# Kernel optimization log

Hardware: AMD Instinct MI355X
Metric: run time of the kernel (lower is better)

## Reference

```python
import jax, jax.numpy as jnp
import numpy as np

B, N, DIM, HEADS = 1, 4096, 1024, 16
HEAD_DIM = DIM // HEADS
SCALE = HEAD_DIM ** -0.5
GRID = 64  # GRID*GRID == N, power-of-2 Hilbert grid


def _hilbert_d2xy(n, d):
    # standard Hilbert curve distance->(x,y), vectorized in numpy
    rx = np.zeros_like(d)
    ry = np.zeros_like(d)
    x = np.zeros_like(d)
    y = np.zeros_like(d)
    t = d.copy()
    s = 1
    while s < n:
        rx = (t // 2) & 1
        ry = (t ^ rx) & 1
        # rotate
        swap = ry == 0
        flip = swap & (rx == 1)
        x_f = np.where(flip, s - 1 - x, x)
        y_f = np.where(flip, s - 1 - y, y)
        x, y = np.where(swap, y_f, x_f), np.where(swap, x_f, y_f)
        x = x + s * rx
        y = y + s * ry
        t = t // 4
        s *= 2
    return x, y


def _hilbert_indices(n_tokens, grid):
    d = np.arange(n_tokens)
    hx, hy = _hilbert_d2xy(grid, d)
    # token at Hilbert distance d lives at row-major position hy*grid+hx
    return (hy * grid + hx).astype(np.int32)


def setup_inputs() -> dict:
    key = jax.random.key(0)
    k1, k2, k3 = jax.random.split(key, 3)
    x = jax.random.normal(k1, (B, N, DIM), dtype=jnp.float32)
    w_qkv = jax.random.normal(k2, (3 * DIM, DIM), dtype=jnp.float32) * (DIM ** -0.5)
    w_out = jax.random.normal(k3, (DIM, DIM), dtype=jnp.float32) * (DIM ** -0.5)
    indices = jnp.asarray(_hilbert_indices(N, GRID))
    return {"x": x, "w_qkv": w_qkv, "w_out": w_out, "indices": indices}


def reference(x, w_qkv, w_out, indices):
    b, n, c = x.shape
    # qkv projection: nn.Linear -> x @ W^T, reshape to [B,N,3,H,Dh]
    qkv = jnp.einsum("bnc,dc->bnd", x, w_qkv).reshape(b, n, 3, HEADS, HEAD_DIM)
    q, k, v = qkv[:, :, 0], qkv[:, :, 1], qkv[:, :, 2]  # each [B,N,H,Dh]
    # Hilbert gather along sequence
    q = q[:, indices]
    k = k[:, indices]
    v = v[:, indices]
    # full softmax attention per head
    scores = jnp.einsum("bnhd,bmhd->bhnm", q, k) * SCALE
    attn = jax.nn.softmax(scores, axis=-1)
    out = jnp.einsum("bhnm,bmhd->bnhd", attn, v)  # [B,N,H,Dh]
    # scatter back to original order
    inv = jnp.argsort(indices)
    out = out[:, inv].reshape(b, n, c)
    return jnp.einsum("bnc,dc->bnd", out, w_out)
```

## Files before the change

kernel.cpp:

```cpp
#include <hip/hip_runtime.h>
#include <stdint.h>

#define NTOK 4096
#define HD 64
#define DIMC 1024

typedef __attribute__((ext_vector_type(8))) short s16x8;
typedef __attribute__((ext_vector_type(4))) float f32x4;

#if __has_builtin(__builtin_amdgcn_exp2f)
#define EXP2(x) __builtin_amdgcn_exp2f(x)
#else
#define EXP2(x) exp2f(x)
#endif

__device__ inline unsigned short f2bf(float f) {
  union { float f; unsigned u; } v; v.f = f;
  unsigned r = v.u + 0x7FFFu + ((v.u >> 16) & 1u);
  return (unsigned short)(r >> 16);
}

__device__ inline unsigned cvt_pk_bf16(float lo, float hi) {
  unsigned r;
  asm("v_cvt_pk_bf16_f32 %0, %1, %2" : "=v"(r) : "v"(lo), "v"(hi));
  return r;
}

__device__ inline float bf2f(unsigned short u) {
  union { unsigned u; float f; } v; v.u = ((unsigned)u) << 16;
  return v.f;
}

__device__ inline void gld16(const void* g, void* s) {
  __builtin_amdgcn_global_load_lds((const __attribute__((address_space(1))) void*)g,
                                   (__attribute__((address_space(3))) void*)s, 16, 0, 0);
}

#define N4_X   1048576
#define N4_WQ  786432
__global__ void cvt_all(const float4* __restrict__ x, const float4* __restrict__ wq,
                        ushort4* __restrict__ xb, ushort4* __restrict__ wqb) {
  int i = blockIdx.x * 256 + threadIdx.x;
  const float4* s; ushort4* d; int off;
  if (i < N4_X) { s = x; d = xb; off = i; }
  else { s = wq; d = wqb; off = i - N4_X; }
  float4 v = s[off];
  ushort4 o;
  o.x = f2bf(v.x); o.y = f2bf(v.y); o.z = f2bf(v.z); o.w = f2bf(v.w);
  d[off] = o;
}

#define QSCALE 0.18033688011112042f
__global__ __launch_bounds__(256) void gemm_qkv(
    const unsigned short* __restrict__ A,
    const unsigned short* __restrict__ B,
    unsigned short* __restrict__ qb,
    unsigned short* __restrict__ kb,
    unsigned short* __restrict__ vtb)
{
  __shared__ unsigned short As[128 * 32];
  __shared__ unsigned short Bs[128 * 32];
  const int t = threadIdx.x;
  const int l = t & 63;
  const int w = t >> 6;
  const int wr = w >> 1, wc = w & 1;
  const int bm = blockIdx.x, bn = blockIdx.y;
  const int K = 1024;

  f32x4 acc[4][4];
#pragma unroll
  for (int m = 0; m < 4; ++m)
#pragma unroll
    for (int n = 0; n < 4; ++n)
#pragma unroll
      for (int r = 0; r < 4; ++r) acc[m][n][r] = 0.f;

  for (int kt = 0; kt < K; kt += 32) {
    __syncthreads();
#pragma unroll
    for (int j = 0; j < 2; ++j) {
      const int o = j * 4096 + t * 16;
      const int row = o >> 6;
      const int cole = (o & 63) >> 1;
      gld16(A + (size_t)(bm * 128 + row) * K + kt + cole, (char*)As + o);
      gld16(B + (size_t)(bn * 128 + row) * K + kt + cole, (char*)Bs + o);
    }
    __syncthreads();
    s16x8 af[4], bfr[4];
    const int cb = (l >> 4) * 16;
#pragma unroll
    for (int m = 0; m < 4; ++m)
      af[m] = *(const s16x8*)((const char*)As + (wr * 64 + m * 16 + (l & 15)) * 64 + cb);
#pragma unroll
    for (int n = 0; n < 4; ++n)
      bfr[n] = *(const s16x8*)((const char*)Bs + (wc * 64 + n * 16 + (l & 15)) * 64 + cb);
#pragma unroll
    for (int m = 0; m < 4; ++m)
#pragma unroll
      for (int n = 0; n < 4; ++n)
        acc[m][n] = __builtin_amdgcn_mfma_f32_16x16x32_bf16(af[m], bfr[n], acc[m][n], 0, 0, 0);
  }

#pragma unroll
  for (int m = 0; m < 4; ++m) {
#pragma unroll
    for (int n = 0; n < 4; ++n) {
#pragma unroll
      for (int r = 0; r < 4; ++r) {
        const int gm = bm * 128 + wr * 64 + m * 16 + (l >> 4) * 4 + r;
        const int gn = bn * 128 + wc * 64 + n * 16 + (l & 15);
        const float val = acc[m][n][r];
        const int part = gn >> 10;
        const int h = (gn >> 6) & 15;
        const int dd = gn & 63;
        if (part == 0)      qb[((size_t)h * NTOK + gm) * HD + dd] = f2bf(val * QSCALE);
        else if (part == 1) kb[((size_t)h * NTOK + gm) * HD + dd] = f2bf(val);
        else                vtb[((size_t)h * HD + dd) * NTOK + gm] = f2bf(val);
      }
    }
  }
}

__global__ __launch_bounds__(128, 4) void fa_split(
    const unsigned short* __restrict__ Q,
    const unsigned short* __restrict__ Kin,
    const unsigned short* __restrict__ Vt,
    unsigned short* __restrict__ Opart,
    float* __restrict__ Lpart)
{
  __shared__ unsigned short Ks[2][32 * 64];
  __shared__ unsigned short Vs[2][64 * 32];

  const int t = threadIdx.x, l = t & 63, w = t >> 6;
  const int g = l >> 4, q = l & 15;
  const int wg = blockIdx.x;
  const int h = wg & 15;
  const int qt = (wg >> 4) & 63;
  const int half = wg >> 10;
  const int q0 = qt * 64 + w * 32;
  const int kbase0 = half * (NTOK / 2);
  const unsigned short* Qh = Q + (size_t)h * NTOK * HD;
  const unsigned short* Kh = Kin + (size_t)h * NTOK * HD;
  const unsigned short* Vh = Vt + (size_t)h * HD * NTOK;

  int offK[2], offV[2];
#pragma unroll
  for (int j = 0; j < 2; ++j) {
    const int o = j * 2048 + t * 16;
    const int rho = o >> 7;
    const int c = o & 127;
    const int n = ((rho & 12) << 1) | ((rho & 16) >> 2) | (rho & 3);
    offK[j] = n * 128 + (c ^ ((rho & 7) << 4));
    const int rv = o >> 6;
    const int cv = o & 63;
    offV[j] = rv * (NTOK * 2) + (cv ^ (((rv >> 1) & 3) << 4));
  }

  s16x8 qf[2][2];
#pragma unroll
  for (int rb = 0; rb < 2; ++rb)
#pragma unroll
    for (int tq = 0; tq < 2; ++tq)
      qf[rb][tq] = *(const s16x8*)(Qh + (size_t)(q0 + rb * 16 + q) * HD + tq * 32 + g * 8);

  s16x8 ones;
#pragma unroll
  for (int i = 0; i < 8; ++i) ones[i] = (short)0x3F80;

  f32x4 oacc[2][4], lacc[2];
#pragma unroll
  for (int rb = 0; rb < 2; ++rb) {
#pragma unroll
    for (int db = 0; db < 4; ++db)
#pragma unroll
      for (int r = 0; r < 4; ++r) oacc[rb][db][r] = 0.f;
#pragma unroll
    for (int r = 0; r < 4; ++r) lacc[rb][r] = 0.f;
  }

#pragma unroll
  for (int j = 0; j < 2; ++j) {
    const int o = j * 2048 + t * 16;
    gld16((const char*)Kh + (size_t)kbase0 * 128 + offK[j], (char*)Ks[0] + o);
    gld16((const char*)Vh + (size_t)kbase0 * 2 + offV[j], (char*)Vs[0] + o);
  }
  __syncthreads();

  int cur = 0;
  const int NIT = (NTOK / 2) / 32;
  for (int it = 0; it < NIT; ++it) {
    if (it + 1 < NIT) {
      const char* kp = (const char*)Kh + (size_t)(kbase0 + (it + 1) * 32) * 128;
      const char* vp = (const char*)Vh + (size_t)(kbase0 + (it + 1) * 32) * 2;
#pragma unroll
      for (int j = 0; j < 2; ++j) {
        const int o = j * 2048 + t * 16;
        gld16(kp + offK[j], (char*)Ks[cur ^ 1] + o);
        gld16(vp + offV[j], (char*)Vs[cur ^ 1] + o);
      }
      asm volatile("s_waitcnt vmcnt(4)" ::: "memory");
    } else {
      asm volatile("s_waitcnt vmcnt(0)" ::: "memory");
    }
    __builtin_amdgcn_sched_barrier(0);
    __builtin_amdgcn_s_barrier();
    __builtin_amdgcn_sched_barrier(0);

    const char* kb = (const char*)Ks[cur];
    const char* vb = (const char*)Vs[cur];

    f32x4 sc[2][2];
    __builtin_amdgcn_s_setprio(1);
#pragma unroll
    for (int kb2 = 0; kb2 < 2; ++kb2) {
      const int row = kb2 * 16 + q;
      const int swz = (row & 7) << 4;
      s16x8 kf0 = *(const s16x8*)(kb + row * 128 + ((g * 16) ^ swz));
      s16x8 kf1 = *(const s16x8*)(kb + row * 128 + ((64 + g * 16) ^ swz));
#pragma unroll
      for (int rb = 0; rb < 2; ++rb) {
        f32x4 z = {0.f, 0.f, 0.f, 0.f};
        z = __builtin_amdgcn_mfma_f32_16x16x32_bf16(kf0, qf[rb][0], z, 0, 0, 0);
        sc[rb][kb2] = __builtin_amdgcn_mfma_f32_16x16x32_bf16(kf1, qf[rb][1], z, 0, 0, 0);
      }
    }
    __builtin_amdgcn_s_setprio(0);

    union PU { unsigned u[4]; s16x8 v; } pu[2];
#pragma unroll
    for (int rb = 0; rb < 2; ++rb) {
      pu[rb].u[0] = cvt_pk_bf16(EXP2(sc[rb][0][0]), EXP2(sc[rb][0][1]));
      pu[rb].u[1] = cvt_pk_bf16(EXP2(sc[rb][0][2]), EXP2(sc[rb][0][3]));
      pu[rb].u[2] = cvt_pk_bf16(EXP2(sc[rb][1][0]), EXP2(sc[rb][1][1]));
      pu[rb].u[3] = cvt_pk_bf16(EXP2(sc[rb][1][2]), EXP2(sc[rb][1][3]));
    }

    __builtin_amdgcn_s_setprio(1);
    const int vswz = ((q >> 1) & 3) << 4;
#pragma unroll
    for (int db = 0; db < 4; ++db) {
      const int row = db * 16 + q;
      s16x8 vf = *(const s16x8*)(vb + row * 64 + ((g * 16) ^ vswz));
#pragma unroll
      for (int rb = 0; rb < 2; ++rb)
        oacc[rb][db] = __builtin_amdgcn_mfma_f32_16x16x32_bf16(vf, pu[rb].v, oacc[rb][db], 0, 0, 0);
    }
#pragma unroll
    for (int rb = 0; rb < 2; ++rb)
      lacc[rb] = __builtin_amdgcn_mfma_f32_16x16x32_bf16(ones, pu[rb].v, lacc[rb], 0, 0, 0);
    __builtin_amdgcn_s_setprio(0);

    __builtin_amdgcn_sched_barrier(0);
    __builtin_amdgcn_s_barrier();
    __builtin_amdgcn_sched_barrier(0);
    cur ^= 1;
  }

  const size_t pbase = ((size_t)(half * 16 + h) * NTOK);
#pragma unroll
  for (int rb = 0; rb < 2; ++rb) {
    const int nn = q0 + rb * 16 + q;
#pragma unroll
    for (int db = 0; db < 4; ++db) {
      uint2 pr;
      pr.x = cvt_pk_bf16(oacc[rb][db][0], oacc[rb][db][1]);
      pr.y = cvt_pk_bf16(oacc[rb][db][2], oacc[rb][db][3]);
      *(uint2*)(Opart + (pbase + nn) * HD + db * 16 + g * 4) = pr;
    }
    if (g == 0) Lpart[pbase + nn] = lacc[rb][0];
  }
}

__global__ __launch_bounds__(256) void fa_combine(
    const unsigned short* __restrict__ Opart,
    const float* __restrict__ Lpart,
    unsigned short* __restrict__ O)
{
  const int tid = blockIdx.x * 256 + threadIdx.x;
  const int d4 = tid & 15;
  const int n = (tid >> 4) & 4095;
  const int h = tid >> 16;
  const size_t stride = (size_t)16 * NTOK * HD;
  const size_t e0 = ((size_t)h * NTOK + n) * HD + d4 * 4;
  ushort4 a = *(const ushort4*)(Opart + e0);
  ushort4 b = *(const ushort4*)(Opart + e0 + stride);
  const float inv = 1.f / (Lpart[(size_t)h * NTOK + n] + Lpart[(size_t)16 * NTOK + (size_t)h * NTOK + n]);
  ushort4 o;
  o.x = f2bf((bf2f(a.x) + bf2f(b.x)) * inv);
  o.y = f2bf((bf2f(a.y) + bf2f(b.y)) * inv);
  o.z = f2bf((bf2f(a.z) + bf2f(b.z)) * inv);
  o.w = f2bf((bf2f(a.w) + bf2f(b.w)) * inv);
  *(ushort4*)(O + (size_t)n * DIMC + h * HD + d4 * 4) = o;
}

__global__ __launch_bounds__(256) void gemm_out(
    const unsigned short* __restrict__ A,
    const float* __restrict__ wout,
    float* __restrict__ outf)
{
  __shared__ unsigned short As[128 * 32];
  __shared__ unsigned short Bs[128 * 32];
  const int t = threadIdx.x;
  const int l = t & 63;
  const int w = t >> 6;
  const int wr = w >> 1, wc = w & 1;
  const int bm = blockIdx.x, bn = blockIdx.y;

  f32x4 acc[4][4];
#pragma unroll
  for (int m = 0; m < 4; ++m)
#pragma unroll
    for (int n = 0; n < 4; ++n)
#pragma unroll
      for (int r = 0; r < 4; ++r) acc[m][n][r] = 0.f;

  for (int kt = 0; kt < 1024; kt += 32) {
    __syncthreads();
#pragma unroll
    for (int j = 0; j < 2; ++j) {
      const int o = j * 4096 + t * 16;
      const int row = o >> 6;
      const int cole = (o & 63) >> 1;
      gld16(A + (size_t)(bm * 128 + row) * 1024 + kt + cole, (char*)As + o);
      const float* bsrc = wout + (size_t)(bn * 128 + row) * 1024 + kt + cole;
      float4 b0 = *(const float4*)bsrc;
      float4 b1 = *(const float4*)(bsrc + 4);
      union PB { unsigned u[4]; s16x8 v; } pb;
      pb.u[0] = cvt_pk_bf16(b0.x, b0.y);
      pb.u[1] = cvt_pk_bf16(b0.z, b0.w);
      pb.u[2] = cvt_pk_bf16(b1.x, b1.y);
      pb.u[3] = cvt_pk_bf16(b1.z, b1.w);
      *(s16x8*)((char*)Bs + o) = pb.v;
    }
    __syncthreads();
    s16x8 af[4], bfr[4];
    const int cb = (l >> 4) * 16;
#pragma unroll
    for (int m = 0; m < 4; ++m)
      af[m] = *(const s16x8*)((const char*)As + (wr * 64 + m * 16 + (l & 15)) * 64 + cb);
#pragma unroll
    for (int n = 0; n < 4; ++n)
      bfr[n] = *(const s16x8*)((const char*)Bs + (wc * 64 + n * 16 + (l & 15)) * 64 + cb);
#pragma unroll
    for (int m = 0; m < 4; ++m)
#pragma unroll
      for (int n = 0; n < 4; ++n)
        acc[m][n] = __builtin_amdgcn_mfma_f32_16x16x32_bf16(af[m], bfr[n], acc[m][n], 0, 0, 0);
  }

#pragma unroll
  for (int m = 0; m < 4; ++m)
#pragma unroll
    for (int n = 0; n < 4; ++n)
#pragma unroll
      for (int r = 0; r < 4; ++r) {
        const int gm = bm * 128 + wr * 64 + m * 16 + (l >> 4) * 4 + r;
        const int gn = bn * 128 + wc * 64 + n * 16 + (l & 15);
        outf[(size_t)gm * 1024 + gn] = acc[m][n][r];
      }
}

extern "C" void kernel_launch(void* const* d_in, const int* in_sizes, int n_in,
                              void* d_out, int out_size, void* d_ws, size_t ws_size,
                              hipStream_t stream) {
  const float* x    = (const float*)d_in[0];
  const float* wqkv = (const float*)d_in[1];
  const float* wout = (const float*)d_in[2];
  float* out = (float*)d_out;
  char* ws = (char*)d_ws;

  unsigned short* Opart = (unsigned short*)(ws);
  unsigned short* xb    = (unsigned short*)(ws);
  unsigned short* wqkvb = (unsigned short*)(ws + 8388608);
  float*          Lp    = (float*)(ws + 16777216);
  unsigned short* Qb    = (unsigned short*)(ws + 17825792);
  unsigned short* Kb    = (unsigned short*)(ws + 26214400);
  unsigned short* Vtb   = (unsigned short*)(ws + 34603008);
  unsigned short* aob   = Qb;

  cvt_all<<<7168, 256, 0, stream>>>((const float4*)x, (const float4*)wqkv,
                                    (ushort4*)xb, (ushort4*)wqkvb);

  gemm_qkv<<<dim3(32, 24), 256, 0, stream>>>(xb, wqkvb, Qb, Kb, Vtb);

  fa_split<<<2048, 128, 0, stream>>>(Qb, Kb, Vtb, Opart, Lp);

  fa_combine<<<4096, 256, 0, stream>>>(Opart, Lp, aob);

  gemm_out<<<dim3(32, 8), 256, 0, stream>>>(aob, wout, out);
}
```

Baseline: 166.8 us.

## Fuse split-KV combine into attention kernel via last-arriver atomic flag

Removes the separate fa_combine launch. Each split-attention block now fences its partial output and increments a per-(head, query-tile) counter, and the second block to arrive merges both halves and writes the bf16 attention output directly. This saves a kernel launch and lets the combine overlap with other attention blocks. In exchange it adds a memset, atomics and thread fences, and it moves the output buffer to a new workspace region so it no longer aliases Q.

```diff
diff --git a/kernel.cpp b/kernel.cpp
--- a/kernel.cpp
+++ b/kernel.cpp
@@ -126,10 +126,13 @@
     const unsigned short* __restrict__ Kin,
     const unsigned short* __restrict__ Vt,
     unsigned short* __restrict__ Opart,
-    float* __restrict__ Lpart)
+    float* __restrict__ Lpart,
+    int* __restrict__ flags,
+    unsigned short* __restrict__ aob)
 {
   __shared__ unsigned short Ks[2][32 * 64];
   __shared__ unsigned short Vs[2][64 * 32];
+  __shared__ int sOld;
 
   const int t = threadIdx.x, l = t & 63, w = t >> 6;
   const int g = l >> 4, q = l & 15;
@@ -269,28 +272,33 @@
     }
     if (g == 0) Lpart[pbase + nn] = lacc[rb][0];
   }
-}
-
-__global__ __launch_bounds__(256) void fa_combine(
-    const unsigned short* __restrict__ Opart,
-    const float* __restrict__ Lpart,
-    unsigned short* __restrict__ O)
-{
-  const int tid = blockIdx.x * 256 + threadIdx.x;
-  const int d4 = tid & 15;
-  const int n = (tid >> 4) & 4095;
-  const int h = tid >> 16;
-  const size_t stride = (size_t)16 * NTOK * HD;
-  const size_t e0 = ((size_t)h * NTOK + n) * HD + d4 * 4;
-  ushort4 a = *(const ushort4*)(Opart + e0);
-  ushort4 b = *(const ushort4*)(Opart + e0 + stride);
-  const float inv = 1.f / (Lpart[(size_t)h * NTOK + n] + Lpart[(size_t)16 * NTOK + (size_t)h * NTOK + n]);
-  ushort4 o;
-  o.x = f2bf((bf2f(a.x) + bf2f(b.x)) * inv);
-  o.y = f2bf((bf2f(a.y) + bf2f(b.y)) * inv);
-  o.z = f2bf((bf2f(a.z) + bf2f(b.z)) * inv);
-  o.w = f2bf((bf2f(a.w) + bf2f(b.w)) * inv);
-  *(ushort4*)(O + (size_t)n * DIMC + h * HD + d4 * 4) = o;
+
+  __threadfence();
+  __syncthreads();
+  if (t == 0) sOld = atomicAdd(&flags[(h << 6) | qt], 1);
+  __syncthreads();
+  if (sOld == 1) {
+    __threadfence();
+    const int q0b = qt * 64;
+    const size_t s1 = (size_t)16 * NTOK * HD;
+    const int nl = t >> 1;
+    const int nn = q0b + nl;
+    const float inv = 1.f / (Lpart[(size_t)h * NTOK + nn] +
+                             Lpart[(size_t)16 * NTOK + (size_t)h * NTOK + nn]);
+    const size_t ebase = ((size_t)h * NTOK + nn) * HD;
+#pragma unroll
+    for (int k2 = 0; k2 < 8; ++k2) {
+      const int c4 = (t & 1) * 8 + k2;
+      ushort4 p0 = *(const ushort4*)(Opart + ebase + c4 * 4);
+      ushort4 p1 = *(const ushort4*)(Opart + ebase + s1 + c4 * 4);
+      ushort4 o;
+      o.x = f2bf((bf2f(p0.x) + bf2f(p1.x)) * inv);
+      o.y = f2bf((bf2f(p0.y) + bf2f(p1.y)) * inv);
+      o.z = f2bf((bf2f(p0.z) + bf2f(p1.z)) * inv);
+      o.w = f2bf((bf2f(p0.w) + bf2f(p1.w)) * inv);
+      *(ushort4*)(aob + (size_t)nn * DIMC + h * HD + c4 * 4) = o;
+    }
+  }
 }
 
 __global__ __launch_bounds__(256) void gemm_out(
@@ -373,19 +381,20 @@
   unsigned short* xb    = (unsigned short*)(ws);
   unsigned short* wqkvb = (unsigned short*)(ws + 8388608);
   float*          Lp    = (float*)(ws + 16777216);
+  int*            flags = (int*)(ws + 17301504);
   unsigned short* Qb    = (unsigned short*)(ws + 17825792);
   unsigned short* Kb    = (unsigned short*)(ws + 26214400);
   unsigned short* Vtb   = (unsigned short*)(ws + 34603008);
-  unsigned short* aob   = Qb;
+  unsigned short* aob   = (unsigned short*)(ws + 42991616);
+
+  hipMemsetAsync(flags, 0, 4096, stream);
 
   cvt_all<<<7168, 256, 0, stream>>>((const float4*)x, (const float4*)wqkv,
                                     (ushort4*)xb, (ushort4*)wqkvb);
 
   gemm_qkv<<<dim3(32, 24), 256, 0, stream>>>(xb, wqkvb, Qb, Kb, Vtb);
 
-  fa_split<<<2048, 128, 0, stream>>>(Qb, Kb, Vtb, Opart, Lp);
-
-  fa_combine<<<4096, 256, 0, stream>>>(Opart, Lp, aob);
+  fa_split<<<2048, 128, 0, stream>>>(Qb, Kb, Vtb, Opart, Lp, flags, aob);
 
   gemm_out<<<dim3(32, 8), 256, 0, stream>>>(aob, wout, out);
 }
```

Measured after the change: 370.6 us. 122% more time.
